# Kernel tuning notes

Measured on AMD Instinct MI355X. Metric: run time of the kernel, lower is better.

The kernel has to match this reference:

```python
import jax, jax.numpy as jnp
import numpy as np

N = 8192      # collocation points
H = 128       # hidden width of the stream-function MLP


def setup_inputs() -> dict:
    key = jax.random.key(0)
    ks = jax.random.split(key, 9)
    s = lambda fan_in: 1.0 / np.sqrt(fan_in)
    return {
        "x":  jax.random.normal(ks[0], (N, 3), dtype=jnp.float32),
        "W1": jax.random.normal(ks[1], (3, H), dtype=jnp.float32) * s(3),
        "b1": jnp.zeros((H,), dtype=jnp.float32),
        "W2": jax.random.normal(ks[2], (H, H), dtype=jnp.float32) * s(H),
        "b2": jnp.zeros((H,), dtype=jnp.float32),
        "W3": jax.random.normal(ks[3], (H, H), dtype=jnp.float32) * s(H),
        "b3": jnp.zeros((H,), dtype=jnp.float32),
        "W4": jax.random.normal(ks[4], (H, 1), dtype=jnp.float32) * s(H),
        "b4": jnp.zeros((1,), dtype=jnp.float32),
        "nu": jnp.float32(1.0),
    }


def reference(x, W1, b1, W2, b2, W3, b3, W4, b4, nu):
    # psi: scalar stream function of a single sample xi = (x, y, t)
    def psi(xi):
        h = jnp.tanh(xi @ W1 + b1)
        h = jnp.tanh(h @ W2 + b2)
        h = jnp.tanh(h @ W3 + b3)
        return (h @ W4 + b4)[0]

    # vorticity w = dv/dx - du/dy = -(psi_xx + psi_yy)
    def w_fn(xi):
        Hpsi = jax.hessian(psi)(xi)          # [3,3]
        return -(Hpsi[0, 0] + Hpsi[1, 1])

    def per_sample(xi):
        g = jax.grad(psi)(xi)                # dpsi: [3]
        u = g[1]
        v = -g[0]
        dw = jax.grad(w_fn)(xi)              # [dwdx, dwdy, dwdt]
        Hw = jax.hessian(w_fn)(xi)           # 4th-order derivs of psi
        lapw = Hw[0, 0] + Hw[1, 1]
        nse = dw[2] + dw[0] * u + dw[1] * v - nu * lapw
        return jnp.stack([u, v]), nse

    f, NSE = jax.vmap(per_sample)(x)         # f: [N,2], NSE: [N]
    return f, NSE
```

## Files before the change

kernel.cpp:

```cpp
#include <hip/hip_runtime.h>
#include <hip/hip_bf16.h>

#define NSAMP 8192
#define HD 128
#define NC 18
#define SB 8
#define NCOLS 144
#define KSTR 136

typedef __attribute__((ext_vector_type(8))) short bf16x8;
typedef __attribute__((ext_vector_type(4))) float f32x4;
typedef float f2 __attribute__((ext_vector_type(2)));


__device__ __forceinline__ unsigned packf2(f2 v) {
    __hip_bfloat162 h = __float22bfloat162_rn(float2{v.x, v.y});
    return *(unsigned*)&h;
}
__device__ __forceinline__ f2 unpk(unsigned r) {
    f2 v;
    v.x = __uint_as_float(r << 16);
    v.y = __uint_as_float(r & 0xffff0000u);
    return v;
}

__device__ __forceinline__ void jmul2(const f2* __restrict__ p,
                                      const f2* __restrict__ q,
                                      f2* __restrict__ r) {
    r[0]  = p[0]*q[0];
    r[1]  = p[0]*q[1]  + p[1]*q[0];
    r[2]  = p[0]*q[2]  + p[2]*q[0];
    r[3]  = p[0]*q[3]  + p[3]*q[0];
    r[4]  = p[0]*q[4]  + p[4]*q[0]  + p[1]*q[1];
    r[5]  = p[0]*q[5]  + p[5]*q[0]  + p[1]*q[2]  + p[2]*q[1];
    r[6]  = p[0]*q[6]  + p[6]*q[0]  + p[2]*q[2];
    r[7]  = p[0]*q[7]  + p[7]*q[0]  + p[1]*q[3]  + p[3]*q[1];
    r[8]  = p[0]*q[8]  + p[8]*q[0]  + p[2]*q[3]  + p[3]*q[2];
    r[9]  = p[0]*q[9]  + p[9]*q[0]  + p[1]*q[4]  + p[4]*q[1];
    r[10] = p[0]*q[10] + p[10]*q[0] + p[1]*q[5]  + p[5]*q[1] + p[2]*q[4] + p[4]*q[2];
    r[11] = p[0]*q[11] + p[11]*q[0] + p[1]*q[6]  + p[6]*q[1] + p[2]*q[5] + p[5]*q[2];
    r[12] = p[0]*q[12] + p[12]*q[0] + p[2]*q[6]  + p[6]*q[2];
    r[13] = p[0]*q[13] + p[13]*q[0] + p[1]*q[7]  + p[7]*q[1] + p[3]*q[4] + p[4]*q[3];
    r[14] = p[0]*q[14] + p[14]*q[0] + p[2]*q[8]  + p[8]*q[2] + p[3]*q[6] + p[6]*q[3];
    r[15] = p[0]*q[15] + p[15]*q[0] + p[1]*q[9]  + p[9]*q[1] + p[4]*q[4];
    r[16] = p[0]*q[16] + p[16]*q[0] + p[1]*q[11] + p[11]*q[1] + p[2]*q[10] + p[10]*q[2]
          + p[4]*q[6]  + p[6]*q[4]  + p[5]*q[5];
    r[17] = p[0]*q[17] + p[17]*q[0] + p[2]*q[12] + p[12]*q[2] + p[6]*q[6];
}

__device__ __forceinline__ void tanh_jet2(const f2* __restrict__ f,
                                          f2* __restrict__ out) {
    f2 y;  y.x = tanhf(f[0].x);  y.y = tanhf(f[0].y);
    const f2 one = {1.0f, 1.0f};
    const f2 s  = one - y*y;
    const f2 t2 = -y*s;
    const f2 t3 = s*(y*y - 0.3333333333333333f);
    const f2 t4 = y*s*(one + one - 3.0f*y*y) * 0.3333333333333333f;
    f2 p[NC], A[NC], B[NC];
    p[0] = (f2)0.0f;
#pragma unroll
    for (int i = 1; i < NC; ++i) p[i] = f[i];
    A[0] = t3;
#pragma unroll
    for (int i = 1; i < NC; ++i) A[i] = t4 * p[i];
    jmul2(p, A, B);  B[0] += t2;
    jmul2(p, B, A);  A[0] += s;
    jmul2(p, A, out); out[0] += y;
}

__global__ __launch_bounds__(512, 4)
void hydro_main(const float* __restrict__ x,
                const float* __restrict__ W1, const float* __restrict__ b1,
                const float* __restrict__ W2, const float* __restrict__ b2,
                const float* __restrict__ W3, const float* __restrict__ b3,
                const float* __restrict__ W4, const float* __restrict__ nu_p,
                float* __restrict__ out) {
    __shared__ __align__(16) unsigned short Hl[NCOLS * KSTR];
    __shared__ float psis[NCOLS];

    const int tid = threadIdx.x;
    const int wv  = tid >> 6;
    const int ln  = tid & 63;
    const int s0  = blockIdx.x * SB;

    {
        const int s  = tid >> 6;
        const int jp = tid & 63;
        const float xs = x[3 * (s0 + s) + 0];
        const float ys = x[3 * (s0 + s) + 1];
        const float ts = x[3 * (s0 + s) + 2];
        const int j0 = 2 * jp;
        const f2 wx = *(const f2*)&W1[j0];
        const f2 wy = *(const f2*)&W1[HD + j0];
        const f2 wt = *(const f2*)&W1[2 * HD + j0];
        const f2 bb = *(const f2*)&b1[j0];
        f2 f[NC], h[NC];
#pragma unroll
        for (int c = 0; c < NC; ++c) f[c] = (f2)0.0f;
        f[0] = wx * xs + wy * ys + wt * ts + bb;
        f[1] = wx; f[2] = wy; f[3] = wt;
        tanh_jet2(f, h);
#pragma unroll
        for (int c = 0; c < NC; ++c)
            *(unsigned*)&Hl[(s * NC + c) * KSTR + j0] = packf2(h[c]);
    }
    __syncthreads();

    const int half = wv & 1;
    const int ntb  = half * 4;
    const int mg   = wv >> 1;
    const int mr0  = mg * 32 + (ln & 15);
    const int koff = (ln >> 4) * 8;

#pragma unroll 1
    for (int L = 0; L < 2; ++L) {
        const float* __restrict__ W = L ? W3 : W2;
        f32x4 acc[2][5];
#pragma unroll
        for (int mt = 0; mt < 2; ++mt)
#pragma unroll
            for (int t = 0; t < 5; ++t) acc[mt][t] = (f32x4)0.0f;

#pragma unroll 1
        for (int ks = 0; ks < 4; ++ks) {
            const int kb = ks * 32 + koff;
            union { uint4 u; bf16x8 v; } a0, a1;
            a0.u.x = packf2(f2{W[(kb + 0) * HD + mr0], W[(kb + 1) * HD + mr0]});
            a0.u.y = packf2(f2{W[(kb + 2) * HD + mr0], W[(kb + 3) * HD + mr0]});
            a0.u.z = packf2(f2{W[(kb + 4) * HD + mr0], W[(kb + 5) * HD + mr0]});
            a0.u.w = packf2(f2{W[(kb + 6) * HD + mr0], W[(kb + 7) * HD + mr0]});
            a1.u.x = packf2(f2{W[(kb + 0) * HD + mr0 + 16], W[(kb + 1) * HD + mr0 + 16]});
            a1.u.y = packf2(f2{W[(kb + 2) * HD + mr0 + 16], W[(kb + 3) * HD + mr0 + 16]});
            a1.u.z = packf2(f2{W[(kb + 4) * HD + mr0 + 16], W[(kb + 5) * HD + mr0 + 16]});
            a1.u.w = packf2(f2{W[(kb + 6) * HD + mr0 + 16], W[(kb + 7) * HD + mr0 + 16]});
#pragma unroll
            for (int t = 0; t < 5; ++t) {
                const int n = (ntb + t) * 16 + (ln & 15);
                const bf16x8 Bf = *(const bf16x8*)&Hl[n * KSTR + kb];
                acc[0][t] = __builtin_amdgcn_mfma_f32_16x16x32_bf16(a0.v, Bf, acc[0][t], 0, 0, 0);
                acc[1][t] = __builtin_amdgcn_mfma_f32_16x16x32_bf16(a1.v, Bf, acc[1][t], 0, 0, 0);
            }
        }
        __syncthreads();
#pragma unroll
        for (int t = 0; t < 5; ++t) {
            const int n  = (ntb + t) * 16 + (ln & 15);
            const int m0 = mg * 32 + (ln >> 4) * 4;
            uint2 w0, w1;
            w0.x = packf2(f2{acc[0][t].x, acc[0][t].y});
            w0.y = packf2(f2{acc[0][t].z, acc[0][t].w});
            w1.x = packf2(f2{acc[1][t].x, acc[1][t].y});
            w1.y = packf2(f2{acc[1][t].z, acc[1][t].w});
            *(uint2*)&Hl[n * KSTR + m0]      = w0;
            *(uint2*)&Hl[n * KSTR + m0 + 16] = w1;
        }
        __syncthreads();
        if (tid < 256) {
            const float* bL = L ? b3 : b2;
            const int s  = tid >> 5;
            const int q  = tid & 31;
            const int j0 = 4 * q;
            f2 fa[NC], fb[NC], ha[NC], hb[NC];
#pragma unroll
            for (int c = 0; c < NC; ++c) {
                const uint2 u = *(const uint2*)&Hl[(s * NC + c) * KSTR + j0];
                fa[c] = unpk(u.x);
                fb[c] = unpk(u.y);
            }
            fa[0] += *(const f2*)&bL[j0];
            fb[0] += *(const f2*)&bL[j0 + 2];
            tanh_jet2(fa, ha);
            tanh_jet2(fb, hb);
#pragma unroll
            for (int c = 0; c < NC; ++c) {
                uint2 w;
                w.x = packf2(ha[c]);
                w.y = packf2(hb[c]);
                *(uint2*)&Hl[(s * NC + c) * KSTR + j0] = w;
            }
        }
        __syncthreads();
    }

    if (tid < NCOLS) {
        float acc = 0.0f;
#pragma unroll
        for (int kk = 0; kk < 16; ++kk) {
            const uint4 q = *(const uint4*)&Hl[tid * KSTR + kk * 8];
            const int k = kk * 8;
            const f2 e0 = unpk(q.x), e1 = unpk(q.y), e2 = unpk(q.z), e3 = unpk(q.w);
            acc = fmaf(e0.x, W4[k + 0], acc);
            acc = fmaf(e0.y, W4[k + 1], acc);
            acc = fmaf(e1.x, W4[k + 2], acc);
            acc = fmaf(e1.y, W4[k + 3], acc);
            acc = fmaf(e2.x, W4[k + 4], acc);
            acc = fmaf(e2.y, W4[k + 5], acc);
            acc = fmaf(e3.x, W4[k + 6], acc);
            acc = fmaf(e3.y, W4[k + 7], acc);
        }
        psis[tid] = acc;
    }
    __syncthreads();

    if (tid < SB) {
        const float* p = &psis[tid * NC];
        const float nu = nu_p[0];
        const float u  = p[2];
        const float v  = -p[1];
        const float wx = -(6.0f * p[9]  + 2.0f * p[11]);
        const float wy = -(2.0f * p[10] + 6.0f * p[12]);
        const float wt = -(2.0f * p[13] + 2.0f * p[14]);
        const float lapw = -(24.0f * p[15] + 8.0f * p[16] + 24.0f * p[17]);
        const float nse  = wt + wx * u + wy * v - nu * lapw;
        const int gi = s0 + tid;
        out[2 * gi]         = u;
        out[2 * gi + 1]     = v;
        out[2 * NSAMP + gi] = nse;
    }
}

extern "C" void kernel_launch(void* const* d_in, const int* in_sizes, int n_in,
                              void* d_out, int out_size, void* d_ws, size_t ws_size,
                              hipStream_t stream) {
    const float* x  = (const float*)d_in[0];
    const float* W1 = (const float*)d_in[1];
    const float* b1 = (const float*)d_in[2];
    const float* W2 = (const float*)d_in[3];
    const float* b2 = (const float*)d_in[4];
    const float* W3 = (const float*)d_in[5];
    const float* b3 = (const float*)d_in[6];
    const float* W4 = (const float*)d_in[7];
    const float* nu = (const float*)d_in[9];
    float* out = (float*)d_out;

    hipLaunchKernelGGL(hydro_main, dim3(NSAMP / SB), dim3(512), 0, stream,
                       x, W1, b1, W2, b2, W3, b3, W4, nu, out);
}
```

Measured before the change: 105.7 us.

## Pre-transpose weights to bf16 workspace and re-split MFMA work per wave

```diff
diff --git a/kernel.cpp b/kernel.cpp
--- a/kernel.cpp
+++ b/kernel.cpp
@@ -68,12 +68,25 @@
     jmul2(p, A, out); out[0] += y;
 }
 
-__global__ __launch_bounds__(512, 4)
+__global__ __launch_bounds__(256)
+void transpose_w(const float* __restrict__ W2, const float* __restrict__ W3,
+                 unsigned* __restrict__ wsT) {
+    const int id = blockIdx.x * 256 + threadIdx.x;
+    if (id >= 2 * HD * (HD / 2)) return;
+    const int L  = id / (HD * (HD / 2));
+    const int r  = id % (HD * (HD / 2));
+    const int j  = r / (HD / 2);
+    const int kp = r % (HD / 2);
+    const float* W = L ? W3 : W2;
+    wsT[id] = packf2(f2{W[(2 * kp) * HD + j], W[(2 * kp + 1) * HD + j]});
+}
+
+__global__ __launch_bounds__(512, 2)
 void hydro_main(const float* __restrict__ x,
                 const float* __restrict__ W1, const float* __restrict__ b1,
-                const float* __restrict__ W2, const float* __restrict__ b2,
-                const float* __restrict__ W3, const float* __restrict__ b3,
+                const float* __restrict__ b2, const float* __restrict__ b3,
                 const float* __restrict__ W4, const float* __restrict__ nu_p,
+                const unsigned short* __restrict__ wsT,
                 float* __restrict__ out) {
     __shared__ __align__(16) unsigned short Hl[NCOLS * KSTR];
     __shared__ float psis[NCOLS];
@@ -106,53 +119,61 @@
     }
     __syncthreads();
 
-    const int half = wv & 1;
-    const int ntb  = half * 4;
-    const int mg   = wv >> 1;
-    const int mr0  = mg * 32 + (ln & 15);
+    const int lr   = ln & 15;
     const int koff = (ln >> 4) * 8;
 
 #pragma unroll 1
     for (int L = 0; L < 2; ++L) {
-        const float* __restrict__ W = L ? W3 : W2;
-        f32x4 acc[2][5];
-#pragma unroll
-        for (int mt = 0; mt < 2; ++mt)
-#pragma unroll
-            for (int t = 0; t < 5; ++t) acc[mt][t] = (f32x4)0.0f;
-
-#pragma unroll 1
+        const unsigned short* __restrict__ WT = wsT + L * HD * HD;
+        bf16x8 Af[8][4];
+#pragma unroll
+        for (int mt = 0; mt < 8; ++mt)
+#pragma unroll
+            for (int ks = 0; ks < 4; ++ks)
+                Af[mt][ks] = *(const bf16x8*)&WT[(mt * 16 + lr) * HD + ks * 32 + koff];
+
+        f32x4 acc0[8];
+#pragma unroll
+        for (int mt = 0; mt < 8; ++mt) acc0[mt] = (f32x4)0.0f;
+#pragma unroll
         for (int ks = 0; ks < 4; ++ks) {
-            const int kb = ks * 32 + koff;
-            union { uint4 u; bf16x8 v; } a0, a1;
-            a0.u.x = packf2(f2{W[(kb + 0) * HD + mr0], W[(kb + 1) * HD + mr0]});
-            a0.u.y = packf2(f2{W[(kb + 2) * HD + mr0], W[(kb + 3) * HD + mr0]});
-            a0.u.z = packf2(f2{W[(kb + 4) * HD + mr0], W[(kb + 5) * HD + mr0]});
-            a0.u.w = packf2(f2{W[(kb + 6) * HD + mr0], W[(kb + 7) * HD + mr0]});
-            a1.u.x = packf2(f2{W[(kb + 0) * HD + mr0 + 16], W[(kb + 1) * HD + mr0 + 16]});
-            a1.u.y = packf2(f2{W[(kb + 2) * HD + mr0 + 16], W[(kb + 3) * HD + mr0 + 16]});
-            a1.u.z = packf2(f2{W[(kb + 4) * HD + mr0 + 16], W[(kb + 5) * HD + mr0 + 16]});
-            a1.u.w = packf2(f2{W[(kb + 6) * HD + mr0 + 16], W[(kb + 7) * HD + mr0 + 16]});
-#pragma unroll
-            for (int t = 0; t < 5; ++t) {
-                const int n = (ntb + t) * 16 + (ln & 15);
-                const bf16x8 Bf = *(const bf16x8*)&Hl[n * KSTR + kb];
-                acc[0][t] = __builtin_amdgcn_mfma_f32_16x16x32_bf16(a0.v, Bf, acc[0][t], 0, 0, 0);
-                acc[1][t] = __builtin_amdgcn_mfma_f32_16x16x32_bf16(a1.v, Bf, acc[1][t], 0, 0, 0);
+            const bf16x8 B0 = *(const bf16x8*)&Hl[(wv * 16 + lr) * KSTR + ks * 32 + koff];
+#pragma unroll
+            for (int mt = 0; mt < 8; ++mt)
+                acc0[mt] = __builtin_amdgcn_mfma_f32_16x16x32_bf16(Af[mt][ks], B0, acc0[mt], 0, 0, 0);
+        }
+        f32x4 acc1[8];
+        if (wv == 0) {
+#pragma unroll
+            for (int mt = 0; mt < 8; ++mt) acc1[mt] = (f32x4)0.0f;
+#pragma unroll
+            for (int ks = 0; ks < 4; ++ks) {
+                const bf16x8 B1 = *(const bf16x8*)&Hl[(128 + lr) * KSTR + ks * 32 + koff];
+#pragma unroll
+                for (int mt = 0; mt < 8; ++mt)
+                    acc1[mt] = __builtin_amdgcn_mfma_f32_16x16x32_bf16(Af[mt][ks], B1, acc1[mt], 0, 0, 0);
             }
         }
         __syncthreads();
 #pragma unroll
-        for (int t = 0; t < 5; ++t) {
-            const int n  = (ntb + t) * 16 + (ln & 15);
-            const int m0 = mg * 32 + (ln >> 4) * 4;
-            uint2 w0, w1;
-            w0.x = packf2(f2{acc[0][t].x, acc[0][t].y});
-            w0.y = packf2(f2{acc[0][t].z, acc[0][t].w});
-            w1.x = packf2(f2{acc[1][t].x, acc[1][t].y});
-            w1.y = packf2(f2{acc[1][t].z, acc[1][t].w});
-            *(uint2*)&Hl[n * KSTR + m0]      = w0;
-            *(uint2*)&Hl[n * KSTR + m0 + 16] = w1;
+        for (int mt = 0; mt < 8; ++mt) {
+            const int n = wv * 16 + lr;
+            const int m = mt * 16 + (ln >> 4) * 4;
+            uint2 w;
+            w.x = packf2(f2{acc0[mt].x, acc0[mt].y});
+            w.y = packf2(f2{acc0[mt].z, acc0[mt].w});
+            *(uint2*)&Hl[n * KSTR + m] = w;
+        }
+        if (wv == 0) {
+#pragma unroll
+            for (int mt = 0; mt < 8; ++mt) {
+                const int n = 128 + lr;
+                const int m = mt * 16 + (ln >> 4) * 4;
+                uint2 w;
+                w.x = packf2(f2{acc1[mt].x, acc1[mt].y});
+                w.y = packf2(f2{acc1[mt].z, acc1[mt].w});
+                *(uint2*)&Hl[n * KSTR + m] = w;
+            }
         }
         __syncthreads();
         if (tid < 256) {
@@ -233,6 +254,9 @@
     const float* nu = (const float*)d_in[9];
     float* out = (float*)d_out;
 
+    unsigned* wsT = (unsigned*)d_ws;
+    hipLaunchKernelGGL(transpose_w, dim3(64), dim3(256), 0, stream, W2, W3, wsT);
     hipLaunchKernelGGL(hydro_main, dim3(NSAMP / SB), dim3(512), 0, stream,
-                       x, W1, b1, W2, b2, W3, b3, W4, nu, out);
-}
+                       x, W1, b1, b2, b3, W4, nu,
+                       (const unsigned short*)d_ws, out);
+}
```

New measurement: 160.9 us. 1.52x slower.
